# Kernel tuning notes

Measured on AMD Instinct MI355X. Metric: run time of the kernel, lower is better.

Reference implementation:

```python
import jax, jax.numpy as jnp
import numpy as np

RADIUS = 0.2
NSAMPLE = 32
NPOINT = 2048
EPS = 1e-5


def setup_inputs() -> dict:
    key = jax.random.key(0)
    ks = jax.random.split(key, 6)
    B, N, C = 8, 8192, 64
    xyz = jax.random.uniform(ks[0], (B, N, 3), dtype=jnp.float32)
    features = jax.random.normal(ks[1], (B, C, N), dtype=jnp.float32)
    W1 = jax.random.normal(ks[2], (64, 67), dtype=jnp.float32) * 0.1
    W2 = jax.random.normal(ks[3], (64, 64), dtype=jnp.float32) * 0.1
    W3 = jax.random.normal(ks[4], (128, 64), dtype=jnp.float32) * 0.1
    return {
        'xyz': xyz, 'features': features,
        'W1': W1, 'g1': jnp.ones((64,), jnp.float32), 'b1': jnp.zeros((64,), jnp.float32),
        'W2': W2, 'g2': jnp.ones((64,), jnp.float32), 'b2': jnp.zeros((64,), jnp.float32),
        'W3': W3, 'g3': jnp.ones((128,), jnp.float32), 'b3': jnp.zeros((128,), jnp.float32),
    }


def furthest_point_sample(xyz, npoint):
    # xyz: (B, N, 3) -> (B, npoint) int32 indices, first index is 0 (CUDA FPS convention)
    B, N, _ = xyz.shape
    idxs0 = jnp.zeros((B, npoint), dtype=jnp.int32)
    dists0 = jnp.full((B, N), 1e10, dtype=xyz.dtype)
    last0 = jnp.zeros((B,), dtype=jnp.int32)

    def body(i, state):
        idxs, dists, last = state
        last_pt = xyz[jnp.arange(B), last]                      # (B, 3)
        d = jnp.sum((xyz - last_pt[:, None, :]) ** 2, axis=-1)  # (B, N)
        dists = jnp.minimum(dists, d)
        nxt = jnp.argmax(dists, axis=-1).astype(jnp.int32)
        idxs = idxs.at[:, i].set(nxt)
        return (idxs, dists, nxt)

    idxs, _, _ = jax.lax.fori_loop(1, npoint, body, (idxs0, dists0, last0))
    return idxs


def ball_query(xyz, new_xyz, radius, nsample):
    # Returns (B, S, nsample) int32: first `nsample` points within radius of each
    # query center, padded with the first in-ball index (pointnet2 convention).
    N = xyz.shape[1]
    d2 = jnp.sum((new_xyz[:, :, None, :] - xyz[:, None, :, :]) ** 2, axis=-1)  # (B,S,N)
    key = jnp.where(d2 < radius * radius, jnp.arange(N, dtype=jnp.int32), N)
    neg_vals, _ = jax.lax.top_k(-key, nsample)   # k smallest keys = earliest in-ball indices
    cand = -neg_vals                             # (B, S, nsample)
    first = cand[..., :1]
    return jnp.where(cand < N, cand, first)


def reference(xyz, features, W1, g1, b1, W2, g2, b2, W3, g3, b3):
    B = xyz.shape[0]
    fps_idx = furthest_point_sample(xyz, NPOINT)              # (B, S)
    new_xyz = xyz[jnp.arange(B)[:, None], fps_idx]            # (B, S, 3)

    idx = ball_query(xyz, new_xyz, RADIUS, NSAMPLE)           # (B, S, ns)
    bb = jnp.arange(B)[:, None, None]
    grouped_xyz = xyz[bb, idx] - new_xyz[:, :, None, :]       # (B, S, ns, 3) relative coords
    grouped_f = features.transpose(0, 2, 1)[bb, idx]          # (B, S, ns, C)
    g = jnp.concatenate([grouped_xyz, grouped_f], axis=-1)    # (B, S, ns, 3+C)
    g = g.transpose(0, 3, 1, 2)                               # (B, 3+C, S, ns)

    for W, ga, be in ((W1, g1, b1), (W2, g2, b2), (W3, g3, b3)):
        h = jnp.einsum('oc,bcsn->bosn', W, g)                 # 1x1 conv
        mu = h.mean(axis=(0, 2, 3), keepdims=True)            # training-mode BN stats
        var = h.var(axis=(0, 2, 3), keepdims=True)
        h = (h - mu) / jnp.sqrt(var + EPS)
        g = jax.nn.relu(h * ga[None, :, None, None] + be[None, :, None, None])

    feats = g.max(axis=-1)                                    # (B, mlp[-1], S)
    return new_xyz, feats
```

## Files before the change

### kernel.cpp

```cpp
#include <hip/hip_runtime.h>
#include <hip/hip_bf16.h>
#include <stdint.h>

#define NB 8
#define NN 8192
#define NC 64
#define NS 2048
#define NK 32
#define NCOL (NB*NS*NK)

typedef float v2f __attribute__((ext_vector_type(2)));

__device__ __forceinline__ unsigned short f2bf(float x) {
    union { float f; unsigned u; } c; c.f = x;
    unsigned r = c.u + 0x7fffu + ((c.u >> 16) & 1u);
    return (unsigned short)(r >> 16);
}
__device__ __forceinline__ float bf2f(unsigned v16) {
    union { float f; unsigned u; } c; c.u = v16 << 16;
    return c.f;
}

template<int CTRL>
__device__ __forceinline__ unsigned long long dpp_max_u64(unsigned long long key) {
    int olo = __builtin_amdgcn_update_dpp(0, (int)(unsigned)key,        CTRL, 0xf, 0xf, true);
    int ohi = __builtin_amdgcn_update_dpp(0, (int)(unsigned)(key >> 32), CTRL, 0xf, 0xf, true);
    unsigned long long ok = ((unsigned long long)(unsigned)ohi << 32) | (unsigned)olo;
    return ok > key ? ok : key;
}
template<int CTRL>
__device__ __forceinline__ float dpp_add_f32(float x) {
    int o = __builtin_amdgcn_update_dpp(0, __float_as_int(x), CTRL, 0xf, 0xf, true);
    return x + __int_as_float(o);
}
template<int CTRL>
__device__ __forceinline__ float dpp_max_f32(float x) {
    int o = __builtin_amdgcn_update_dpp(__float_as_int(x), __float_as_int(x), CTRL, 0xf, 0xf, false);
    return fmaxf(x, __int_as_float(o));
}
template<int CTRL>
__device__ __forceinline__ float dpp_min_f32(float x) {
    int o = __builtin_amdgcn_update_dpp(__float_as_int(x), __float_as_int(x), CTRL, 0xf, 0xf, false);
    return fminf(x, __int_as_float(o));
}
template<int CTRL>
__device__ __forceinline__ unsigned dpp_max_u32(unsigned x) {
    int o = __builtin_amdgcn_update_dpp((int)x, (int)x, CTRL, 0xf, 0xf, false);
    unsigned ou = (unsigned)o;
    return x > ou ? x : ou;
}
template<int CTRL, int RM>
__device__ __forceinline__ unsigned dpp_add_u32(unsigned x) {
    int o = __builtin_amdgcn_update_dpp(0, (int)x, CTRL, RM, 0xf, true);
    return x + (unsigned)o;
}
__device__ __forceinline__ float wave_red_min(float x) {
    x = dpp_min_f32<0x111>(x); x = dpp_min_f32<0x112>(x);
    x = dpp_min_f32<0x114>(x); x = dpp_min_f32<0x118>(x);
    x = dpp_min_f32<0x142>(x); x = dpp_min_f32<0x143>(x);
    return __int_as_float(__builtin_amdgcn_readlane(__float_as_int(x), 63));
}
__device__ __forceinline__ float wave_red_max(float x) {
    x = dpp_max_f32<0x111>(x); x = dpp_max_f32<0x112>(x);
    x = dpp_max_f32<0x114>(x); x = dpp_max_f32<0x118>(x);
    x = dpp_max_f32<0x142>(x); x = dpp_max_f32<0x143>(x);
    return __int_as_float(__builtin_amdgcn_readlane(__float_as_int(x), 63));
}
__device__ __forceinline__ v2f relu2(v2f v) {
    v.x = fmaxf(v.x, 0.f); v.y = fmaxf(v.y, 0.f); return v;
}

__device__ __forceinline__ unsigned expand_bits10(unsigned v) {
    v = (v * 0x00010001u) & 0xFF0000FFu;
    v = (v * 0x00000101u) & 0x0F00F00Fu;
    v = (v * 0x00000011u) & 0xC30C30C3u;
    v = (v * 0x00000005u) & 0x49249249u;
    return v;
}
__global__ __launch_bounds__(1024) void sort_kernel(const float* __restrict__ xyz,
    float4* __restrict__ sorted)
{
    __shared__ unsigned cnt[2048];
    __shared__ unsigned codes[NN];
    __shared__ unsigned wsum[16];
    const int b = blockIdx.x;
    const int tid = threadIdx.x;
    const int w = tid >> 6;
    const int lane = tid & 63;
    const float* xb = xyz + (size_t)b * NN * 3;
    cnt[tid] = 0; cnt[tid + 1024] = 0;
    __syncthreads();
    for (int p = tid; p < NN; p += 1024) {
        float x = xb[3*p+0], y = xb[3*p+1], z = xb[3*p+2];
        int qx = (int)(x * 1024.f); qx = qx < 0 ? 0 : (qx > 1023 ? 1023 : qx);
        int qy = (int)(y * 1024.f); qy = qy < 0 ? 0 : (qy > 1023 ? 1023 : qy);
        int qz = (int)(z * 1024.f); qz = qz < 0 ? 0 : (qz > 1023 ? 1023 : qz);
        unsigned m = expand_bits10((unsigned)qx)
                   | (expand_bits10((unsigned)qy) << 1)
                   | (expand_bits10((unsigned)qz) << 2);
        unsigned bk = m >> 19;
        codes[p] = bk;
        atomicAdd(&cnt[bk], 1u);
    }
    __syncthreads();
    unsigned c0 = cnt[2*tid], c1 = cnt[2*tid+1];
    unsigned s = c0 + c1;
    unsigned v = s;
    v = dpp_add_u32<0x111, 0xf>(v);
    v = dpp_add_u32<0x112, 0xf>(v);
    v = dpp_add_u32<0x114, 0xf>(v);
    v = dpp_add_u32<0x118, 0xf>(v);
    v = dpp_add_u32<0x142, 0xa>(v);
    v = dpp_add_u32<0x143, 0xc>(v);
    if (lane == 63) wsum[w] = v;
    __syncthreads();
    unsigned wbase = 0;
#pragma unroll
    for (int j = 0; j < 15; ++j) {
        unsigned t = wsum[j];
        wbase += (j < w) ? t : 0u;
    }
    unsigned excl = wbase + v - s;
    cnt[2*tid]   = excl;
    cnt[2*tid+1] = excl + c0;
    __syncthreads();
    for (int p = tid; p < NN; p += 1024) {
        unsigned bk = codes[p];
        unsigned pos = atomicAdd(&cnt[bk], 1u);
        float4 o;
        o.x = xb[3*p+0]; o.y = xb[3*p+1]; o.z = xb[3*p+2];
        o.w = __int_as_float(p);
        sorted[(size_t)b * NN + pos] = o;
    }
}

__global__ __launch_bounds__(1024) void fps_kernel(const float* __restrict__ xyz,
    const float4* __restrict__ sorted,
    float* __restrict__ new_xyz, float* __restrict__ out_newxyz)
{
#pragma clang fp contract(off)
    const int b = blockIdx.x;
    const int tid = threadIdx.x;
    const int w = tid >> 6;
    const int lane = tid & 63;
    __shared__ float sx[NN], sy[NN], sz[NN];
    __shared__ float s_hist[NS * 3];
    __shared__ unsigned long long s_key[2][16];
    const float4* sp = sorted + (size_t)b * NN + (size_t)w * 512 + lane;
    v2f px[4], py[4], pz[4], dmin[4];
    unsigned plo[8];
    float bnx = 1e30f, bny = 1e30f, bnz = 1e30f;
    float bxx = -1e30f, bxy = -1e30f, bxz = -1e30f;
#pragma unroll
    for (int m = 0; m < 4; ++m) {
        float4 a = sp[128*m];
        float4 c = sp[128*m + 64];
        px[m].x = a.x; px[m].y = c.x;
        py[m].x = a.y; py[m].y = c.y;
        pz[m].x = a.z; pz[m].y = c.z;
        dmin[m].x = 1e10f; dmin[m].y = 1e10f;
        int ia = __float_as_int(a.w), ic = __float_as_int(c.w);
        plo[2*m]   = ~(unsigned)ia;
        plo[2*m+1] = ~(unsigned)ic;
        sx[ia] = a.x; sy[ia] = a.y; sz[ia] = a.z;
        sx[ic] = c.x; sy[ic] = c.y; sz[ic] = c.z;
        bnx = fminf(bnx, fminf(a.x, c.x)); bxx = fmaxf(bxx, fmaxf(a.x, c.x));
        bny = fminf(bny, fminf(a.y, c.y)); bxy = fmaxf(bxy, fmaxf(a.y, c.y));
        bnz = fminf(bnz, fminf(a.z, c.z)); bxz = fmaxf(bxz, fmaxf(a.z, c.z));
    }
    bnx = wave_red_min(bnx); bny = wave_red_min(bny); bnz = wave_red_min(bnz);
    bxx = wave_red_max(bxx); bxy = wave_red_max(bxy); bxz = wave_red_max(bxz);

    const float* xb = xyz + (size_t)b * NN * 3;
    float lx = xb[0], ly = xb[1], lz = xb[2];
    if (tid == 0) { s_hist[0] = lx; s_hist[1] = ly; s_hist[2] = lz; }
    float ckv = 1e30f;
    unsigned cklo = 0u;
    __syncthreads();

    for (int i = 1; i < NS; ++i) {
        float cdx = fmaxf(fmaxf(bnx - lx, lx - bxx), 0.f);
        float cdy = fmaxf(fmaxf(bny - ly, ly - bxy), 0.f);
        float cdz = fmaxf(fmaxf(bnz - lz, lz - bxz), 0.f);
        float lb = (cdx*cdx + cdy*cdy) + cdz*cdz;
        if (!(lb >= ckv)) {
            v2f l2x; l2x.x = lx; l2x.y = lx;
            v2f l2y; l2y.x = ly; l2y.y = ly;
            v2f l2z; l2z.x = lz; l2z.y = lz;
#pragma unroll
            for (int m = 0; m < 4; ++m) {
                v2f dx = px[m] - l2x;
                v2f dy = py[m] - l2y;
                v2f dz = pz[m] - l2z;
                v2f d = (dx*dx + dy*dy) + dz*dz;
                dmin[m].x = fminf(dmin[m].x, d.x);
                dmin[m].y = fminf(dmin[m].y, d.y);
            }
            float bv = fmaxf(
                fmaxf(fmaxf(dmin[0].x, dmin[0].y), fmaxf(dmin[1].x, dmin[1].y)),
                fmaxf(fmaxf(dmin[2].x, dmin[2].y), fmaxf(dmin[3].x, dmin[3].y)));
            float mv = bv;
            mv = dpp_max_f32<0x111>(mv); mv = dpp_max_f32<0x112>(mv);
            mv = dpp_max_f32<0x114>(mv); mv = dpp_max_f32<0x118>(mv);
            mv = dpp_max_f32<0x142>(mv); mv = dpp_max_f32<0x143>(mv);
            const unsigned vmb = (unsigned)__builtin_amdgcn_readlane(__float_as_int(mv), 63);
            const float vmax = __uint_as_float(vmb);
            unsigned cand = 0u;
#pragma unroll
            for (int m = 0; m < 4; ++m) {
                unsigned t0 = (dmin[m].x == vmax) ? plo[2*m]   : 0u;
                unsigned t1 = (dmin[m].y == vmax) ? plo[2*m+1] : 0u;
                unsigned t = t0 > t1 ? t0 : t1;
                cand = cand > t ? cand : t;
            }
            cand = dpp_max_u32<0x111>(cand); cand = dpp_max_u32<0x112>(cand);
            cand = dpp_max_u32<0x114>(cand); cand = dpp_max_u32<0x118>(cand);
            cand = dpp_max_u32<0x142>(cand); cand = dpp_max_u32<0x143>(cand);
            cklo = (unsigned)__builtin_amdgcn_readlane((int)cand, 63);
            ckv = vmax;
        }
        if (lane == 0)
            s_key[i & 1][w] = ((unsigned long long)__float_as_uint(ckv) << 32) | cklo;
        __syncthreads();
        unsigned long long k = s_key[i & 1][lane & 15];
        k = dpp_max_u64<0x111>(k);
        k = dpp_max_u64<0x112>(k);
        k = dpp_max_u64<0x114>(k);
        k = dpp_max_u64<0x118>(k);
        const int ix = ~__builtin_amdgcn_readlane((int)(unsigned)(k & 0xffffffffull), 15);
        lx = sx[ix]; ly = sy[ix]; lz = sz[ix];
        if (tid == 0) {
            s_hist[3*i+0] = lx; s_hist[3*i+1] = ly; s_hist[3*i+2] = lz;
        }
    }
    __syncthreads();
    float* nw = new_xyz + (size_t)b * NS * 3;
    float* ow = out_newxyz + (size_t)b * NS * 3;
    for (int t = tid; t < NS * 3; t += 1024) {
        float v = s_hist[t];
        nw[t] = v; ow[t] = v;
    }
}

__global__ __launch_bounds__(256) void transpose_kernel(const float* __restrict__ f,
    float* __restrict__ ft)
{
    __shared__ float tile[64][65];
    int b = blockIdx.y;
    int p0 = blockIdx.x * 64;
    for (int k = threadIdx.x; k < 64*64; k += 256) {
        int c = k >> 6, p = k & 63;
        tile[c][p] = f[((size_t)b * NC + c) * NN + p0 + p];
    }
    __syncthreads();
    for (int k = threadIdx.x; k < 64*64; k += 256) {
        int p = k >> 6, c = k & 63;
        ft[((size_t)b * NN + p0 + p) * NC + c] = tile[c][p];
    }
}

__global__ __launch_bounds__(256) void ballquery_kernel(const float* __restrict__ xyz,
    const float* __restrict__ new_xyz, int* __restrict__ idx)
{
#pragma clang fp contract(off)
    const int q = blockIdx.x * 4 + (threadIdx.x >> 6);
    const int lane = threadIdx.x & 63;
    const int b = q >> 11;
    const float r2 = (float)(0.2 * 0.2);
    const float* xb = xyz + (size_t)b * NN * 3;
    const float* nx = new_xyz + (size_t)q * 3;
    float qx = nx[0], qy = nx[1], qz = nx[2];
    int cnt = 0, first = -1;
    int* out = idx + (size_t)q * NK;
    for (int base = 0; base < NN; base += 64) {
        int p = base + lane;
        float x = xb[p*3+0], y = xb[p*3+1], z = xb[p*3+2];
        float dx = qx - x, dy = qy - y, dz = qz - z;
        float d2 = (dx*dx + dy*dy) + dz*dz;
        bool in = d2 < r2;
        unsigned long long m = __ballot(in);
        if (m) {
            if (first < 0) first = base + __builtin_ctzll(m);
            if (in) {
                int rank = cnt + __popcll(m & ((1ull << lane) - 1ull));
                if (rank < NK) out[rank] = p;
            }
            cnt += __popcll(m);
            if (cnt >= NK) break;
        }
    }
    for (int k = cnt + lane; k < NK; k += 64) out[k] = first;
}

__global__ __launch_bounds__(256, 2) void layer1_kernel(const float* __restrict__ xyz,
    const float* __restrict__ new_xyz, const int* __restrict__ idx,
    const float* __restrict__ ft, const float* __restrict__ W1,
    unsigned short* __restrict__ h1)
{
    const int col = blockIdx.x * 256 + threadIdx.x;
    const int b = col >> 16;
    const int s = (col >> 5) & 2047;
    const int p = idx[col];
    v2f g[34];
    float* gf = (float*)g;
    {
        const float* nx = new_xyz + ((size_t)(b * NS + s)) * 3;
        const float* xp = xyz + ((size_t)(b * NN + p)) * 3;
        gf[0] = xp[0] - nx[0]; gf[1] = xp[1] - nx[1]; gf[2] = xp[2] - nx[2];
    }
    const float4* fp = (const float4*)(ft + ((size_t)(b * NN + p)) * NC);
#pragma unroll
    for (int c4 = 0; c4 < 16; ++c4) {
        float4 v = fp[c4];
        gf[3 + 4*c4 + 0] = v.x; gf[3 + 4*c4 + 1] = v.y;
        gf[3 + 4*c4 + 2] = v.z; gf[3 + 4*c4 + 3] = v.w;
    }
    gf[67] = 0.f;
    uint4* dst = (uint4*)(h1 + (size_t)col * 64);
#pragma unroll
    for (int half = 0; half < 2; ++half) {
        float h[32];
#pragma unroll 4
        for (int o16 = 0; o16 < 32; ++o16) {
            const float* w = W1 + (half*32 + o16) * 67;
            v2f acc; acc.x = 0.f; acc.y = 0.f;
#pragma unroll
            for (int k = 0; k < 33; ++k) {
                v2f wv; wv.x = w[2*k]; wv.y = w[2*k+1];
                acc = wv * g[k] + acc;
            }
            h[o16] = fmaf(w[66], gf[66], acc.x + acc.y);
        }
#pragma unroll
        for (int k = 0; k < 4; ++k) {
            uint4 v;
            v.x = (unsigned)f2bf(h[8*k+0]) | ((unsigned)f2bf(h[8*k+1]) << 16);
            v.y = (unsigned)f2bf(h[8*k+2]) | ((unsigned)f2bf(h[8*k+3]) << 16);
            v.z = (unsigned)f2bf(h[8*k+4]) | ((unsigned)f2bf(h[8*k+5]) << 16);
            v.w = (unsigned)f2bf(h[8*k+6]) | ((unsigned)f2bf(h[8*k+7]) << 16);
            dst[half*4 + k] = v;
        }
    }
}

__global__ __launch_bounds__(256) void stats_kernel(const unsigned short* __restrict__ h,
    float* __restrict__ sums)
{
    __shared__ float ls[64], lq[64];
    const int tid = threadIdx.x;
    if (tid < 64) { ls[tid] = 0.f; lq[tid] = 0.f; }
    __syncthreads();
    float s[8] = {0,0,0,0,0,0,0,0}, q[8] = {0,0,0,0,0,0,0,0};
    const int gt = blockIdx.x * 256 + tid;
    const int G = gridDim.x * 256;
    const uint4* src = (const uint4*)h;
    const int nvec = NCOL * 8;
    for (int i = gt; i < nvec; i += G) {
        uint4 v = src[i];
        float f0 = bf2f(v.x & 0xffffu), f1 = bf2f(v.x >> 16);
        float f2 = bf2f(v.y & 0xffffu), f3 = bf2f(v.y >> 16);
        float f4 = bf2f(v.z & 0xffffu), f5 = bf2f(v.z >> 16);
        float f6 = bf2f(v.w & 0xffffu), f7 = bf2f(v.w >> 16);
        s[0] += f0; q[0] = fmaf(f0, f0, q[0]);
        s[1] += f1; q[1] = fmaf(f1, f1, q[1]);
        s[2] += f2; q[2] = fmaf(f2, f2, q[2]);
        s[3] += f3; q[3] = fmaf(f3, f3, q[3]);
        s[4] += f4; q[4] = fmaf(f4, f4, q[4]);
        s[5] += f5; q[5] = fmaf(f5, f5, q[5]);
        s[6] += f6; q[6] = fmaf(f6, f6, q[6]);
        s[7] += f7; q[7] = fmaf(f7, f7, q[7]);
    }
    const int obase = (tid & 7) * 8;
#pragma unroll
    for (int j = 0; j < 8; ++j) {
        atomicAdd(&ls[obase + j], s[j]);
        atomicAdd(&lq[obase + j], q[j]);
    }
    __syncthreads();
    if (tid < 64) {
        atomicAdd(&sums[tid*2+0], ls[tid]);
        atomicAdd(&sums[tid*2+1], lq[tid]);
    }
}

__global__ void finalize_kernel(const float* __restrict__ sums,
    const float* __restrict__ gamma, const float* __restrict__ beta,
    float* __restrict__ ab, int nch)
{
    int c = threadIdx.x;
    if (c < nch) {
        const float invM = 1.0f / 524288.0f;
        float mu = sums[c*2] * invM;
        float var = sums[c*2+1] * invM - mu * mu;
        float a = gamma[c] / sqrtf(var + 1e-5f);
        ab[c] = a;
        ab[nch + c] = fmaf(-mu, a, beta[c]);
    }
}

__global__ __launch_bounds__(256, 2) void layer2_kernel(const unsigned short* __restrict__ h1,
    const float* __restrict__ ab1, const float* __restrict__ W2,
    unsigned short* __restrict__ h2)
{
    const int col = blockIdx.x * 256 + threadIdx.x;
    const uint4* src = (const uint4*)(h1 + (size_t)col * 64);
    v2f g[32];
    float* gf = (float*)g;
#pragma unroll
    for (int k = 0; k < 8; ++k) {
        uint4 v = src[k];
        gf[8*k+0] = bf2f(v.x & 0xffffu); gf[8*k+1] = bf2f(v.x >> 16);
        gf[8*k+2] = bf2f(v.y & 0xffffu); gf[8*k+3] = bf2f(v.y >> 16);
        gf[8*k+4] = bf2f(v.z & 0xffffu); gf[8*k+5] = bf2f(v.z >> 16);
        gf[8*k+6] = bf2f(v.w & 0xffffu); gf[8*k+7] = bf2f(v.w >> 16);
    }
    const v2f* a2 = (const v2f*)ab1;
    const v2f* b2 = (const v2f*)(ab1 + 64);
#pragma unroll
    for (int k = 0; k < 32; ++k)
        g[k] = relu2(a2[k] * g[k] + b2[k]);
    uint4* dst = (uint4*)(h2 + (size_t)col * 64);
#pragma unroll
    for (int half = 0; half < 2; ++half) {
        float h[32];
#pragma unroll 4
        for (int o16 = 0; o16 < 32; ++o16) {
            const float* w = W2 + ((half*32 + o16) << 6);
            v2f acc; acc.x = 0.f; acc.y = 0.f;
#pragma unroll
            for (int k = 0; k < 32; ++k) {
                v2f wv; wv.x = w[2*k]; wv.y = w[2*k+1];
                acc = wv * g[k] + acc;
            }
            h[o16] = acc.x + acc.y;
        }
#pragma unroll
        for (int k = 0; k < 4; ++k) {
            uint4 v;
            v.x = (unsigned)f2bf(h[8*k+0]) | ((unsigned)f2bf(h[8*k+1]) << 16);
            v.y = (unsigned)f2bf(h[8*k+2]) | ((unsigned)f2bf(h[8*k+3]) << 16);
            v.z = (unsigned)f2bf(h[8*k+4]) | ((unsigned)f2bf(h[8*k+5]) << 16);
            v.w = (unsigned)f2bf(h[8*k+6]) | ((unsigned)f2bf(h[8*k+7]) << 16);
            dst[half*4 + k] = v;
        }
    }
}

__global__ __launch_bounds__(256, 2) void layer3_kernel(const unsigned short* __restrict__ h2,
    const float* __restrict__ ab2, const float* __restrict__ W3,
    float* __restrict__ hmax, float* __restrict__ hmin, float* __restrict__ sums3)
{
    __shared__ float ls[128], lq[128];
    const int tid = threadIdx.x;
    if (tid < 128) { ls[tid] = 0.f; lq[tid] = 0.f; }
    __syncthreads();
    const int col = blockIdx.x * 256 + tid;
    const int q = col >> 5;
    const uint4* src = (const uint4*)(h2 + (size_t)col * 64);
    v2f g[32];
    float* gf = (float*)g;
#pragma unroll
    for (int k = 0; k < 8; ++k) {
        uint4 v = src[k];
        gf[8*k+0] = bf2f(v.x & 0xffffu); gf[8*k+1] = bf2f(v.x >> 16);
        gf[8*k+2] = bf2f(v.y & 0xffffu); gf[8*k+3] = bf2f(v.y >> 16);
        gf[8*k+4] = bf2f(v.z & 0xffffu); gf[8*k+5] = bf2f(v.z >> 16);
        gf[8*k+6] = bf2f(v.w & 0xffffu); gf[8*k+7] = bf2f(v.w >> 16);
    }
    const v2f* a2 = (const v2f*)ab2;
    const v2f* b2 = (const v2f*)(ab2 + 64);
#pragma unroll
    for (int k = 0; k < 32; ++k)
        g[k] = relu2(a2[k] * g[k] + b2[k]);
    const bool leader = ((tid & 31) == 31);
#pragma unroll 2
    for (int o = 0; o < 128; ++o) {
        const float* w = W3 + (o << 6);
        v2f acc; acc.x = 0.f; acc.y = 0.f;
#pragma unroll
        for (int k = 0; k < 32; ++k) {
            v2f wv; wv.x = w[2*k]; wv.y = w[2*k+1];
            acc = wv * g[k] + acc;
        }
        float hv = acc.x + acc.y;
        float sm = hv, sq = hv*hv, mx = hv, mn = hv;
        sm = dpp_add_f32<0x111>(sm); sq = dpp_add_f32<0x111>(sq);
        mx = dpp_max_f32<0x111>(mx); mn = dpp_min_f32<0x111>(mn);
        sm = dpp_add_f32<0x112>(sm); sq = dpp_add_f32<0x112>(sq);
        mx = dpp_max_f32<0x112>(mx); mn = dpp_min_f32<0x112>(mn);
        sm = dpp_add_f32<0x114>(sm); sq = dpp_add_f32<0x114>(sq);
        mx = dpp_max_f32<0x114>(mx); mn = dpp_min_f32<0x114>(mn);
        sm = dpp_add_f32<0x118>(sm); sq = dpp_add_f32<0x118>(sq);
        mx = dpp_max_f32<0x118>(mx); mn = dpp_min_f32<0x118>(mn);
        sm = dpp_add_f32<0x142>(sm); sq = dpp_add_f32<0x142>(sq);
        mx = dpp_max_f32<0x142>(mx); mn = dpp_min_f32<0x142>(mn);
        if (leader) {
            hmax[(size_t)o * 16384 + q] = mx;
            hmin[(size_t)o * 16384 + q] = mn;
            atomicAdd(&ls[o], sm);
            atomicAdd(&lq[o], sq);
        }
    }
    __syncthreads();
    if (tid < 128) {
        atomicAdd(&sums3[tid*2+0], ls[tid]);
        atomicAdd(&sums3[tid*2+1], lq[tid]);
    }
}

__global__ __launch_bounds__(256) void final_kernel(const float* __restrict__ hmax,
    const float* __restrict__ hmin, const float* __restrict__ ab3,
    float* __restrict__ out)
{
    const int t = blockIdx.x * 256 + threadIdx.x;
    const int s = t & 2047;
    const int o = (t >> 11) & 127;
    const int b = t >> 18;
    const int q = (b << 11) + s;
    float a = ab3[o], c = ab3[128 + o];
    float h = (a >= 0.f) ? hmax[(size_t)o * 16384 + q] : hmin[(size_t)o * 16384 + q];
    out[t] = fmaxf(fmaf(a, h, c), 0.f);
}

extern "C" void kernel_launch(void* const* d_in, const int* in_sizes, int n_in,
                              void* d_out, int out_size, void* d_ws, size_t ws_size,
                              hipStream_t stream) {
    (void)in_sizes; (void)n_in; (void)out_size; (void)ws_size;
    const float* xyz      = (const float*)d_in[0];
    const float* features = (const float*)d_in[1];
    const float* W1 = (const float*)d_in[2];
    const float* g1 = (const float*)d_in[3];
    const float* b1 = (const float*)d_in[4];
    const float* W2 = (const float*)d_in[5];
    const float* g2 = (const float*)d_in[6];
    const float* b2 = (const float*)d_in[7];
    const float* W3 = (const float*)d_in[8];
    const float* g3 = (const float*)d_in[9];
    const float* b3 = (const float*)d_in[10];

    char* ws = (char*)d_ws;
    float*          new_xyz = (float*)(ws + 0);
    int*            idx     = (int*)(ws + 196608);
    float*          ft      = (float*)(ws + 2293760);
    unsigned short* h1      = (unsigned short*)(ws + 19070976);
    unsigned short* h2      = (unsigned short*)(ws + 86179840);
    float*          hmax    = (float*)(ws + 153288704);
    float*          hmin    = (float*)(ws + 161677312);
    float*          sums    = (float*)(ws + 170065920);
    float*          ab      = (float*)(ws + 170067968);
    float* sums1 = sums;        float* ab1 = ab;
    float* sums2 = sums + 128;  float* ab2 = ab + 128;
    float* sums3 = sums + 256;  float* ab3 = ab + 256;

    float4* sorted = (float4*)h1;

    float* out_newxyz = (float*)d_out;
    float* out_feats  = (float*)d_out + 49152;

    hipMemsetAsync(sums, 0, 2048, stream);

    sort_kernel<<<NB, 1024, 0, stream>>>(xyz, sorted);
    fps_kernel<<<NB, 1024, 0, stream>>>(xyz, sorted, new_xyz, out_newxyz);
    transpose_kernel<<<dim3(NN/64, NB), 256, 0, stream>>>(features, ft);
    ballquery_kernel<<<(NB*NS)/4, 256, 0, stream>>>(xyz, new_xyz, idx);
    layer1_kernel<<<NCOL/256, 256, 0, stream>>>(xyz, new_xyz, idx, ft, W1, h1);
    stats_kernel<<<1024, 256, 0, stream>>>(h1, sums1);
    finalize_kernel<<<1, 128, 0, stream>>>(sums1, g1, b1, ab1, 64);
    layer2_kernel<<<NCOL/256, 256, 0, stream>>>(h1, ab1, W2, h2);
    stats_kernel<<<1024, 256, 0, stream>>>(h2, sums2);
    finalize_kernel<<<1, 128, 0, stream>>>(sums2, g2, b2, ab2, 64);
    layer3_kernel<<<NCOL/256, 256, 0, stream>>>(h2, ab2, W3, hmax, hmin, sums3);
    finalize_kernel<<<1, 128, 0, stream>>>(sums3, g3, b3, ab3, 128);
    final_kernel<<<(NB*128*NS)/256, 256, 0, stream>>>(hmax, hmin, ab3, out_feats);
}
```

Before: 2.261 ms.

## Halve FPS block to 8 waves and carry winner coordinates in wave records

The FPS kernel now runs with 512 threads (8 waves), each lane holding 16 points instead of 8. Each wave looks up its own candidate's coordinates inside its bounding-box-gated branch and publishes value, index and xyz in a shared record. The cross-wave reduction then needs only 3 DPP steps over 8 entries and reads the winner's coordinates via readlane, instead of a dependent LDS lookup after the barrier. This shortens the serial per-iteration critical path and barrier cost, at the price of more per-lane work and register pressure. Ties are broken by index first and then by wave id packed into the low bits.

```diff
diff --git a/kernel.cpp b/kernel.cpp
--- a/kernel.cpp
+++ b/kernel.cpp
@@ -8,6 +8,7 @@
 #define NS 2048
 #define NK 32
 #define NCOL (NB*NS*NK)
+#define FW 8
 
 typedef float v2f __attribute__((ext_vector_type(2)));
 
@@ -21,13 +22,6 @@
     return c.f;
 }
 
-template<int CTRL>
-__device__ __forceinline__ unsigned long long dpp_max_u64(unsigned long long key) {
-    int olo = __builtin_amdgcn_update_dpp(0, (int)(unsigned)key,        CTRL, 0xf, 0xf, true);
-    int ohi = __builtin_amdgcn_update_dpp(0, (int)(unsigned)(key >> 32), CTRL, 0xf, 0xf, true);
-    unsigned long long ok = ((unsigned long long)(unsigned)ohi << 32) | (unsigned)olo;
-    return ok > key ? ok : key;
-}
 template<int CTRL>
 __device__ __forceinline__ float dpp_add_f32(float x) {
     int o = __builtin_amdgcn_update_dpp(0, __float_as_int(x), CTRL, 0xf, 0xf, true);
@@ -134,7 +128,7 @@
     }
 }
 
-__global__ __launch_bounds__(1024) void fps_kernel(const float* __restrict__ xyz,
+__global__ __launch_bounds__(512) void fps_kernel(const float* __restrict__ xyz,
     const float4* __restrict__ sorted,
     float* __restrict__ new_xyz, float* __restrict__ out_newxyz)
 {
@@ -145,14 +139,14 @@
     const int lane = tid & 63;
     __shared__ float sx[NN], sy[NN], sz[NN];
     __shared__ float s_hist[NS * 3];
-    __shared__ unsigned long long s_key[2][16];
-    const float4* sp = sorted + (size_t)b * NN + (size_t)w * 512 + lane;
-    v2f px[4], py[4], pz[4], dmin[4];
-    unsigned plo[8];
+    __shared__ float s_rec[2][FW][12];
+    const float4* sp = sorted + (size_t)b * NN + (size_t)w * 1024 + lane;
+    v2f px[8], py[8], pz[8], dmin[8];
+    unsigned plo[16];
     float bnx = 1e30f, bny = 1e30f, bnz = 1e30f;
     float bxx = -1e30f, bxy = -1e30f, bxz = -1e30f;
 #pragma unroll
-    for (int m = 0; m < 4; ++m) {
+    for (int m = 0; m < 8; ++m) {
         float4 a = sp[128*m];
         float4 c = sp[128*m + 64];
         px[m].x = a.x; px[m].y = c.x;
@@ -171,11 +165,20 @@
     bnx = wave_red_min(bnx); bny = wave_red_min(bny); bnz = wave_red_min(bnz);
     bxx = wave_red_max(bxx); bxy = wave_red_max(bxy); bxz = wave_red_max(bxz);
 
+    int rw, roff;
+    if (lane < 8)       { rw = lane;      roff = 0; }
+    else if (lane < 16) { rw = lane - 8;  roff = 2; }
+    else if (lane < 24) { rw = lane - 16; roff = 4; }
+    else                { rw = 0;         roff = 0; }
+    const float* rb0 = &s_rec[0][rw][roff];
+    const float* rb1 = &s_rec[1][rw][roff];
+
     const float* xb = xyz + (size_t)b * NN * 3;
     float lx = xb[0], ly = xb[1], lz = xb[2];
     if (tid == 0) { s_hist[0] = lx; s_hist[1] = ly; s_hist[2] = lz; }
     float ckv = 1e30f;
-    unsigned cklo = 0u;
+    unsigned cki = 0u;
+    float cwx = 0.f, cwy = 0.f, cwz = 0.f;
     __syncthreads();
 
     for (int i = 1; i < NS; ++i) {
@@ -188,7 +191,7 @@
             v2f l2y; l2y.x = ly; l2y.y = ly;
             v2f l2z; l2z.x = lz; l2z.y = lz;
 #pragma unroll
-            for (int m = 0; m < 4; ++m) {
+            for (int m = 0; m < 8; ++m) {
                 v2f dx = px[m] - l2x;
                 v2f dy = py[m] - l2y;
                 v2f dz = pz[m] - l2z;
@@ -196,39 +199,55 @@
                 dmin[m].x = fminf(dmin[m].x, d.x);
                 dmin[m].y = fminf(dmin[m].y, d.y);
             }
-            float bv = fmaxf(
-                fmaxf(fmaxf(dmin[0].x, dmin[0].y), fmaxf(dmin[1].x, dmin[1].y)),
-                fmaxf(fmaxf(dmin[2].x, dmin[2].y), fmaxf(dmin[3].x, dmin[3].y)));
-            float mv = bv;
+            float t0 = fmaxf(fmaxf(dmin[0].x, dmin[0].y), fmaxf(dmin[1].x, dmin[1].y));
+            float t1 = fmaxf(fmaxf(dmin[2].x, dmin[2].y), fmaxf(dmin[3].x, dmin[3].y));
+            float t2 = fmaxf(fmaxf(dmin[4].x, dmin[4].y), fmaxf(dmin[5].x, dmin[5].y));
+            float t3 = fmaxf(fmaxf(dmin[6].x, dmin[6].y), fmaxf(dmin[7].x, dmin[7].y));
+            float mv = fmaxf(fmaxf(t0, t1), fmaxf(t2, t3));
             mv = dpp_max_f32<0x111>(mv); mv = dpp_max_f32<0x112>(mv);
             mv = dpp_max_f32<0x114>(mv); mv = dpp_max_f32<0x118>(mv);
             mv = dpp_max_f32<0x142>(mv); mv = dpp_max_f32<0x143>(mv);
-            const unsigned vmb = (unsigned)__builtin_amdgcn_readlane(__float_as_int(mv), 63);
-            const float vmax = __uint_as_float(vmb);
+            const float vmax = __uint_as_float(
+                (unsigned)__builtin_amdgcn_readlane(__float_as_int(mv), 63));
             unsigned cand = 0u;
 #pragma unroll
-            for (int m = 0; m < 4; ++m) {
-                unsigned t0 = (dmin[m].x == vmax) ? plo[2*m]   : 0u;
-                unsigned t1 = (dmin[m].y == vmax) ? plo[2*m+1] : 0u;
-                unsigned t = t0 > t1 ? t0 : t1;
-                cand = cand > t ? cand : t;
+            for (int m = 0; m < 8; ++m) {
+                unsigned u0 = (dmin[m].x == vmax) ? plo[2*m]   : 0u;
+                unsigned u1 = (dmin[m].y == vmax) ? plo[2*m+1] : 0u;
+                unsigned u = u0 > u1 ? u0 : u1;
+                cand = cand > u ? cand : u;
             }
             cand = dpp_max_u32<0x111>(cand); cand = dpp_max_u32<0x112>(cand);
             cand = dpp_max_u32<0x114>(cand); cand = dpp_max_u32<0x118>(cand);
             cand = dpp_max_u32<0x142>(cand); cand = dpp_max_u32<0x143>(cand);
-            cklo = (unsigned)__builtin_amdgcn_readlane((int)cand, 63);
+            cki = (unsigned)__builtin_amdgcn_readlane((int)cand, 63);
             ckv = vmax;
-        }
-        if (lane == 0)
-            s_key[i & 1][w] = ((unsigned long long)__float_as_uint(ckv) << 32) | cklo;
+            const int ix = (int)(~cki);
+            cwx = sx[ix]; cwy = sy[ix]; cwz = sz[ix];
+        }
+        if (lane == 63) {
+            float* r = (float*)&s_rec[i & 1][w][0];
+            ((unsigned*)r)[0] = __float_as_uint(ckv);
+            ((unsigned*)r)[1] = (cki << 3) | (unsigned)w;
+            r[2] = cwx; r[3] = cwy; r[4] = cwz;
+        }
         __syncthreads();
-        unsigned long long k = s_key[i & 1][lane & 15];
-        k = dpp_max_u64<0x111>(k);
-        k = dpp_max_u64<0x112>(k);
-        k = dpp_max_u64<0x114>(k);
-        k = dpp_max_u64<0x118>(k);
-        const int ix = ~__builtin_amdgcn_readlane((int)(unsigned)(k & 0xffffffffull), 15);
-        lx = sx[ix]; ly = sy[ix]; lz = sz[ix];
+        const float* rp = (i & 1) ? rb1 : rb0;
+        uint2 rec = *(const uint2*)rp;
+        float kv = __uint_as_float(rec.x);
+        float m1 = kv;
+        m1 = dpp_max_f32<0x111>(m1); m1 = dpp_max_f32<0x112>(m1);
+        m1 = dpp_max_f32<0x114>(m1);
+        const float gmax = __uint_as_float(
+            (unsigned)__builtin_amdgcn_readlane(__float_as_int(m1), 7));
+        unsigned c = (lane < 8 && kv == gmax) ? rec.y : 0u;
+        c = dpp_max_u32<0x111>(c); c = dpp_max_u32<0x112>(c);
+        c = dpp_max_u32<0x114>(c);
+        const unsigned kwin = (unsigned)__builtin_amdgcn_readlane((int)c, 7);
+        const int wstar = (int)(kwin & 7u);
+        lx = __uint_as_float((unsigned)__builtin_amdgcn_readlane((int)rec.x, 8 + wstar));
+        ly = __uint_as_float((unsigned)__builtin_amdgcn_readlane((int)rec.y, 8 + wstar));
+        lz = __uint_as_float((unsigned)__builtin_amdgcn_readlane((int)rec.x, 16 + wstar));
         if (tid == 0) {
             s_hist[3*i+0] = lx; s_hist[3*i+1] = ly; s_hist[3*i+2] = lz;
         }
@@ -236,7 +255,7 @@
     __syncthreads();
     float* nw = new_xyz + (size_t)b * NS * 3;
     float* ow = out_newxyz + (size_t)b * NS * 3;
-    for (int t = tid; t < NS * 3; t += 1024) {
+    for (int t = tid; t < NS * 3; t += 512) {
         float v = s_hist[t];
         nw[t] = v; ow[t] = v;
     }
@@ -560,7 +579,7 @@
     hipMemsetAsync(sums, 0, 2048, stream);
 
     sort_kernel<<<NB, 1024, 0, stream>>>(xyz, sorted);
-    fps_kernel<<<NB, 1024, 0, stream>>>(xyz, sorted, new_xyz, out_newxyz);
+    fps_kernel<<<NB, 512, 0, stream>>>(xyz, sorted, new_xyz, out_newxyz);
     transpose_kernel<<<dim3(NN/64, NB), 256, 0, stream>>>(features, ft);
     ballquery_kernel<<<(NB*NS)/4, 256, 0, stream>>>(xyz, new_xyz, idx);
     layer1_kernel<<<NCOL/256, 256, 0, stream>>>(xyz, new_xyz, idx, ft, W1, h1);
```

Result: slower. 2.532 ms (+12.0%).

## Pack two batches per FPS block with 8 waves each and register-held winner coords

Applied to the files above, without the earlier changes.

The FPS kernel now processes two batches per 1024-thread block, so each batch gets 8 waves instead of 16, and each wave holds 1024 points split into two spatially-sorted sub-chunks, each with its own bounding-box prune. The winning point's coordinates are written by the owning lane into a small shared record and broadcast with readlane. This replaces the full 8192-point shared coordinate table and the 64-bit key reduction with a two-pass 32-bit max. The aim is fewer blocks and barriers, finer-grained pruning, and less shared-memory traffic per iteration. In exchange each wave does twice the serial work per iteration, only 4 blocks run, and batches sharing a block are coupled through __syncthreads.

```diff
diff --git a/kernel.cpp b/kernel.cpp
--- a/kernel.cpp
+++ b/kernel.cpp
@@ -21,13 +21,6 @@
     return c.f;
 }
 
-template<int CTRL>
-__device__ __forceinline__ unsigned long long dpp_max_u64(unsigned long long key) {
-    int olo = __builtin_amdgcn_update_dpp(0, (int)(unsigned)key,        CTRL, 0xf, 0xf, true);
-    int ohi = __builtin_amdgcn_update_dpp(0, (int)(unsigned)(key >> 32), CTRL, 0xf, 0xf, true);
-    unsigned long long ok = ((unsigned long long)(unsigned)ohi << 32) | (unsigned)olo;
-    return ok > key ? ok : key;
-}
 template<int CTRL>
 __device__ __forceinline__ float dpp_add_f32(float x) {
     int o = __builtin_amdgcn_update_dpp(0, __float_as_int(x), CTRL, 0xf, 0xf, true);
@@ -134,110 +127,161 @@
     }
 }
 
+#define VMAX6(mv) \
+    mv = dpp_max_f32<0x111>(mv); mv = dpp_max_f32<0x112>(mv); \
+    mv = dpp_max_f32<0x114>(mv); mv = dpp_max_f32<0x118>(mv); \
+    mv = dpp_max_f32<0x142>(mv); mv = dpp_max_f32<0x143>(mv);
+#define UMAX6(cv) \
+    cv = dpp_max_u32<0x111>(cv); cv = dpp_max_u32<0x112>(cv); \
+    cv = dpp_max_u32<0x114>(cv); cv = dpp_max_u32<0x118>(cv); \
+    cv = dpp_max_u32<0x142>(cv); cv = dpp_max_u32<0x143>(cv);
+#define UPD(M) \
+    dx = px[M]-l2x; dy = py[M]-l2y; dz = pz[M]-l2z; \
+    d = (dx*dx + dy*dy) + dz*dz; \
+    dmin[M].x = fminf(dmin[M].x, d.x); dmin[M].y = fminf(dmin[M].y, d.y);
+#define TIE(M) \
+    u = (dmin[M].x == vmax) ? (pidx[M] & 0xffffu) : 0u; cand = cand > u ? cand : u; \
+    u = (dmin[M].y == vmax) ? (pidx[M] >> 16)     : 0u; cand = cand > u ? cand : u;
+#define CSEL(S, M) \
+    e = ((pidx[M] & 0xffffu) == cki##S); iwin##S = iwin##S | e; \
+    wx##S = e ? px[M].x : wx##S; wy##S = e ? py[M].x : wy##S; wz##S = e ? pz[M].x : wz##S; \
+    e = ((pidx[M] >> 16) == cki##S);     iwin##S = iwin##S | e; \
+    wx##S = e ? px[M].y : wx##S; wy##S = e ? py[M].y : wy##S; wz##S = e ? pz[M].y : wz##S;
+#define DO_SUB(S, MA, MB, MC, MD) \
+  { \
+    float cdx = fmaxf(fmaxf(bn##S##x - lx, lx - bx##S##x), 0.f); \
+    float cdy = fmaxf(fmaxf(bn##S##y - ly, ly - bx##S##y), 0.f); \
+    float cdz = fmaxf(fmaxf(bn##S##z - lz, lz - bx##S##z), 0.f); \
+    float lb = (cdx*cdx + cdy*cdy) + cdz*cdz; \
+    if (!(lb >= ckv##S)) {                        \
+      v2f l2x; l2x.x = lx; l2x.y = lx; \
+      v2f l2y; l2y.x = ly; l2y.y = ly; \
+      v2f l2z; l2z.x = lz; l2z.y = lz; \
+      v2f dx, dy, dz, d; \
+      UPD(MA) UPD(MB) UPD(MC) UPD(MD) \
+      float t0 = fmaxf(fmaxf(dmin[MA].x, dmin[MA].y), fmaxf(dmin[MB].x, dmin[MB].y)); \
+      float t1 = fmaxf(fmaxf(dmin[MC].x, dmin[MC].y), fmaxf(dmin[MD].x, dmin[MD].y)); \
+      float mv = fmaxf(t0, t1); \
+      VMAX6(mv) \
+      const float vmax = __uint_as_float( \
+          (unsigned)__builtin_amdgcn_readlane(__float_as_int(mv), 63)); \
+      unsigned cand = 0u, u; \
+      TIE(MA) TIE(MB) TIE(MC) TIE(MD) \
+      UMAX6(cand) \
+      cki##S = (unsigned)__builtin_amdgcn_readlane((int)cand, 63); \
+      ckv##S = vmax; \
+      iwin##S = false;                           \
+      bool e; \
+      CSEL(S, MA) CSEL(S, MB) CSEL(S, MC) CSEL(S, MD) \
+    } \
+    if (lane == 0) { \
+      uint2 kk2; kk2.x = __float_as_uint(ckv##S); kk2.y = (cki##S << 4) | (unsigned)sid##S; \
+      W->kvki[sid##S] = kk2; \
+    } \
+    if (iwin##S) { \
+      W->coord[sid##S]      = wx##S; \
+      W->coord[16 + sid##S] = wy##S; \
+      W->coord[32 + sid##S] = wz##S; \
+    } \
+  }
+
+struct FpsRec { uint2 kvki[16]; float coord[48]; };
+
 __global__ __launch_bounds__(1024) void fps_kernel(const float* __restrict__ xyz,
     const float4* __restrict__ sorted,
     float* __restrict__ new_xyz, float* __restrict__ out_newxyz)
 {
 #pragma clang fp contract(off)
-    const int b = blockIdx.x;
+    const int blk = blockIdx.x;
     const int tid = threadIdx.x;
     const int w = tid >> 6;
     const int lane = tid & 63;
-    __shared__ float sx[NN], sy[NN], sz[NN];
-    __shared__ float s_hist[NS * 3];
-    __shared__ unsigned long long s_key[2][16];
-    const float4* sp = sorted + (size_t)b * NN + (size_t)w * 512 + lane;
-    v2f px[4], py[4], pz[4], dmin[4];
-    unsigned plo[8];
-    float bnx = 1e30f, bny = 1e30f, bnz = 1e30f;
-    float bxx = -1e30f, bxy = -1e30f, bxz = -1e30f;
-#pragma unroll
-    for (int m = 0; m < 4; ++m) {
+    const int bbl = w >> 3;
+    const int ww = w & 7;
+    const int batch = blk * 2 + bbl;
+
+    __shared__ FpsRec s_rec[2][2];
+    __shared__ float s_hist[2][NS * 3];
+
+    const float4* sp = sorted + (size_t)batch * NN + (size_t)ww * 1024 + lane;
+    v2f px[8], py[8], pz[8], dmin[8];
+    unsigned pidx[8];
+    float bn0x = 1e30f, bn0y = 1e30f, bn0z = 1e30f;
+    float bx0x = -1e30f, bx0y = -1e30f, bx0z = -1e30f;
+    float bn1x = 1e30f, bn1y = 1e30f, bn1z = 1e30f;
+    float bx1x = -1e30f, bx1y = -1e30f, bx1z = -1e30f;
+#pragma unroll
+    for (int m = 0; m < 8; ++m) {
         float4 a = sp[128*m];
         float4 c = sp[128*m + 64];
         px[m].x = a.x; px[m].y = c.x;
         py[m].x = a.y; py[m].y = c.y;
         pz[m].x = a.z; pz[m].y = c.z;
         dmin[m].x = 1e10f; dmin[m].y = 1e10f;
-        int ia = __float_as_int(a.w), ic = __float_as_int(c.w);
-        plo[2*m]   = ~(unsigned)ia;
-        plo[2*m+1] = ~(unsigned)ic;
-        sx[ia] = a.x; sy[ia] = a.y; sz[ia] = a.z;
-        sx[ic] = c.x; sy[ic] = c.y; sz[ic] = c.z;
-        bnx = fminf(bnx, fminf(a.x, c.x)); bxx = fmaxf(bxx, fmaxf(a.x, c.x));
-        bny = fminf(bny, fminf(a.y, c.y)); bxy = fmaxf(bxy, fmaxf(a.y, c.y));
-        bnz = fminf(bnz, fminf(a.z, c.z)); bxz = fmaxf(bxz, fmaxf(a.z, c.z));
-    }
-    bnx = wave_red_min(bnx); bny = wave_red_min(bny); bnz = wave_red_min(bnz);
-    bxx = wave_red_max(bxx); bxy = wave_red_max(bxy); bxz = wave_red_max(bxz);
-
-    const float* xb = xyz + (size_t)b * NN * 3;
+        unsigned ia = (unsigned)__float_as_int(a.w), ic = (unsigned)__float_as_int(c.w);
+        pidx[m] = (8192u - ia) | ((8192u - ic) << 16);
+        if (m < 4) {
+            bn0x = fminf(bn0x, fminf(a.x, c.x)); bx0x = fmaxf(bx0x, fmaxf(a.x, c.x));
+            bn0y = fminf(bn0y, fminf(a.y, c.y)); bx0y = fmaxf(bx0y, fmaxf(a.y, c.y));
+            bn0z = fminf(bn0z, fminf(a.z, c.z)); bx0z = fmaxf(bx0z, fmaxf(a.z, c.z));
+        } else {
+            bn1x = fminf(bn1x, fminf(a.x, c.x)); bx1x = fmaxf(bx1x, fmaxf(a.x, c.x));
+            bn1y = fminf(bn1y, fminf(a.y, c.y)); bx1y = fmaxf(bx1y, fmaxf(a.y, c.y));
+            bn1z = fminf(bn1z, fminf(a.z, c.z)); bx1z = fmaxf(bx1z, fmaxf(a.z, c.z));
+        }
+    }
+    bn0x = wave_red_min(bn0x); bn0y = wave_red_min(bn0y); bn0z = wave_red_min(bn0z);
+    bx0x = wave_red_max(bx0x); bx0y = wave_red_max(bx0y); bx0z = wave_red_max(bx0z);
+    bn1x = wave_red_min(bn1x); bn1y = wave_red_min(bn1y); bn1z = wave_red_min(bn1z);
+    bx1x = wave_red_max(bx1x); bx1y = wave_red_max(bx1y); bx1z = wave_red_max(bx1z);
+
+    const int roff = (lane < 16) ? lane * 8 : 128 + (lane - 16) * 4;
+    const char* rb0 = (const char*)&s_rec[0][bbl] + roff;
+    const char* rb1 = (const char*)&s_rec[1][bbl] + roff;
+
+    const float* xb = xyz + (size_t)batch * NN * 3;
     float lx = xb[0], ly = xb[1], lz = xb[2];
-    if (tid == 0) { s_hist[0] = lx; s_hist[1] = ly; s_hist[2] = lz; }
-    float ckv = 1e30f;
-    unsigned cklo = 0u;
-    __syncthreads();
+    if (lane == 0 && ww == 0) {
+        s_hist[bbl][0] = lx; s_hist[bbl][1] = ly; s_hist[bbl][2] = lz;
+    }
+    float ckv0 = 1e30f, ckv1 = 1e30f;
+    unsigned cki0 = 0u, cki1 = 0u;
+    bool iwin0 = false, iwin1 = false;
+    float wx0 = 0, wy0 = 0, wz0 = 0, wx1 = 0, wy1 = 0, wz1 = 0;
+    const int sid0 = ww * 2, sid1 = ww * 2 + 1;
 
     for (int i = 1; i < NS; ++i) {
-        float cdx = fmaxf(fmaxf(bnx - lx, lx - bxx), 0.f);
-        float cdy = fmaxf(fmaxf(bny - ly, ly - bxy), 0.f);
-        float cdz = fmaxf(fmaxf(bnz - lz, lz - bxz), 0.f);
-        float lb = (cdx*cdx + cdy*cdy) + cdz*cdz;
-        if (!(lb >= ckv)) {
-            v2f l2x; l2x.x = lx; l2x.y = lx;
-            v2f l2y; l2y.x = ly; l2y.y = ly;
-            v2f l2z; l2z.x = lz; l2z.y = lz;
-#pragma unroll
-            for (int m = 0; m < 4; ++m) {
-                v2f dx = px[m] - l2x;
-                v2f dy = py[m] - l2y;
-                v2f dz = pz[m] - l2z;
-                v2f d = (dx*dx + dy*dy) + dz*dz;
-                dmin[m].x = fminf(dmin[m].x, d.x);
-                dmin[m].y = fminf(dmin[m].y, d.y);
-            }
-            float bv = fmaxf(
-                fmaxf(fmaxf(dmin[0].x, dmin[0].y), fmaxf(dmin[1].x, dmin[1].y)),
-                fmaxf(fmaxf(dmin[2].x, dmin[2].y), fmaxf(dmin[3].x, dmin[3].y)));
-            float mv = bv;
-            mv = dpp_max_f32<0x111>(mv); mv = dpp_max_f32<0x112>(mv);
-            mv = dpp_max_f32<0x114>(mv); mv = dpp_max_f32<0x118>(mv);
-            mv = dpp_max_f32<0x142>(mv); mv = dpp_max_f32<0x143>(mv);
-            const unsigned vmb = (unsigned)__builtin_amdgcn_readlane(__float_as_int(mv), 63);
-            const float vmax = __uint_as_float(vmb);
-            unsigned cand = 0u;
-#pragma unroll
-            for (int m = 0; m < 4; ++m) {
-                unsigned t0 = (dmin[m].x == vmax) ? plo[2*m]   : 0u;
-                unsigned t1 = (dmin[m].y == vmax) ? plo[2*m+1] : 0u;
-                unsigned t = t0 > t1 ? t0 : t1;
-                cand = cand > t ? cand : t;
-            }
-            cand = dpp_max_u32<0x111>(cand); cand = dpp_max_u32<0x112>(cand);
-            cand = dpp_max_u32<0x114>(cand); cand = dpp_max_u32<0x118>(cand);
-            cand = dpp_max_u32<0x142>(cand); cand = dpp_max_u32<0x143>(cand);
-            cklo = (unsigned)__builtin_amdgcn_readlane((int)cand, 63);
-            ckv = vmax;
-        }
-        if (lane == 0)
-            s_key[i & 1][w] = ((unsigned long long)__float_as_uint(ckv) << 32) | cklo;
+        FpsRec* W = &s_rec[i & 1][bbl];
+        DO_SUB(0, 0, 1, 2, 3)
+        DO_SUB(1, 4, 5, 6, 7)
         __syncthreads();
-        unsigned long long k = s_key[i & 1][lane & 15];
-        k = dpp_max_u64<0x111>(k);
-        k = dpp_max_u64<0x112>(k);
-        k = dpp_max_u64<0x114>(k);
-        k = dpp_max_u64<0x118>(k);
-        const int ix = ~__builtin_amdgcn_readlane((int)(unsigned)(k & 0xffffffffull), 15);
-        lx = sx[ix]; ly = sy[ix]; lz = sz[ix];
-        if (tid == 0) {
-            s_hist[3*i+0] = lx; s_hist[3*i+1] = ly; s_hist[3*i+2] = lz;
-        }
-    }
-    __syncthreads();
-    float* nw = new_xyz + (size_t)b * NS * 3;
-    float* ow = out_newxyz + (size_t)b * NS * 3;
-    for (int t = tid; t < NS * 3; t += 1024) {
-        float v = s_hist[t];
+        const char* rp = (i & 1) ? rb1 : rb0;
+        uint2 kk; kk.x = 0u; kk.y = 0u;
+        unsigned rcbits = 0u;
+        if (lane < 16) kk = *(const uint2*)rp;
+        else rcbits = *(const unsigned*)rp;
+        unsigned mkv = (lane < 16) ? kk.x : 0u;
+        mkv = dpp_max_u32<0x111>(mkv); mkv = dpp_max_u32<0x112>(mkv);
+        mkv = dpp_max_u32<0x114>(mkv); mkv = dpp_max_u32<0x118>(mkv);
+        const unsigned gkv = (unsigned)__builtin_amdgcn_readlane((int)mkv, 15);
+        unsigned c = (lane < 16 && kk.x == gkv) ? kk.y : 0u;
+        c = dpp_max_u32<0x111>(c); c = dpp_max_u32<0x112>(c);
+        c = dpp_max_u32<0x114>(c); c = dpp_max_u32<0x118>(c);
+        const unsigned kwin = (unsigned)__builtin_amdgcn_readlane((int)c, 15);
+        const int sub = (int)(kwin & 15u);
+        lx = __uint_as_float((unsigned)__builtin_amdgcn_readlane((int)rcbits, 16 + sub));
+        ly = __uint_as_float((unsigned)__builtin_amdgcn_readlane((int)rcbits, 32 + sub));
+        lz = __uint_as_float((unsigned)__builtin_amdgcn_readlane((int)rcbits, 48 + sub));
+        if (lane == 0 && ww == 0) {
+            s_hist[bbl][3*i+0] = lx; s_hist[bbl][3*i+1] = ly; s_hist[bbl][3*i+2] = lz;
+        }
+    }
+    __syncthreads();
+    const float* hf = (const float*)s_hist;
+    float* nw = new_xyz + (size_t)(blk * 2) * NS * 3;
+    float* ow = out_newxyz + (size_t)(blk * 2) * NS * 3;
+    for (int t = tid; t < 2 * NS * 3; t += 1024) {
+        float v = hf[t];
         nw[t] = v; ow[t] = v;
     }
 }
@@ -560,7 +604,7 @@
     hipMemsetAsync(sums, 0, 2048, stream);
 
     sort_kernel<<<NB, 1024, 0, stream>>>(xyz, sorted);
-    fps_kernel<<<NB, 1024, 0, stream>>>(xyz, sorted, new_xyz, out_newxyz);
+    fps_kernel<<<NB/2, 1024, 0, stream>>>(xyz, sorted, new_xyz, out_newxyz);
     transpose_kernel<<<dim3(NN/64, NB), 256, 0, stream>>>(features, ft);
     ballquery_kernel<<<(NB*NS)/4, 256, 0, stream>>>(xyz, new_xyz, idx);
     layer1_kernel<<<NCOL/256, 256, 0, stream>>>(xyz, new_xyz, idx, ft, W1, h1);
```

New measurement: 5.659 ms. 150% more time.

## Have each wave publish its winner coordinates instead of staging all points in LDS

Applied to the files above, without the earlier changes.

FPS no longer copies all 8192 points into shared-memory coordinate arrays. Each wave now publishes its winning distance, a packed index key and the winner's xyz in a small double-buffered record. Wave 0 reduces the 16 records with 32-bit DPP max and readlanes, then writes the chosen point to the history buffer. Every thread reads the new point back after a second barrier. This removes the 64-bit key reduction and the large LDS footprint, but adds a second __syncthreads per iteration and serialises the cross-wave reduction through wave 0.

```diff
diff --git a/kernel.cpp b/kernel.cpp
--- a/kernel.cpp
+++ b/kernel.cpp
@@ -21,13 +21,6 @@
     return c.f;
 }
 
-template<int CTRL>
-__device__ __forceinline__ unsigned long long dpp_max_u64(unsigned long long key) {
-    int olo = __builtin_amdgcn_update_dpp(0, (int)(unsigned)key,        CTRL, 0xf, 0xf, true);
-    int ohi = __builtin_amdgcn_update_dpp(0, (int)(unsigned)(key >> 32), CTRL, 0xf, 0xf, true);
-    unsigned long long ok = ((unsigned long long)(unsigned)ohi << 32) | (unsigned)olo;
-    return ok > key ? ok : key;
-}
 template<int CTRL>
 __device__ __forceinline__ float dpp_add_f32(float x) {
     int o = __builtin_amdgcn_update_dpp(0, __float_as_int(x), CTRL, 0xf, 0xf, true);
@@ -134,6 +127,17 @@
     }
 }
 
+#define VMAX6(mv) \
+    mv = dpp_max_f32<0x111>(mv); mv = dpp_max_f32<0x112>(mv); \
+    mv = dpp_max_f32<0x114>(mv); mv = dpp_max_f32<0x118>(mv); \
+    mv = dpp_max_f32<0x142>(mv); mv = dpp_max_f32<0x143>(mv);
+#define UMAX6(cv) \
+    cv = dpp_max_u32<0x111>(cv); cv = dpp_max_u32<0x112>(cv); \
+    cv = dpp_max_u32<0x114>(cv); cv = dpp_max_u32<0x118>(cv); \
+    cv = dpp_max_u32<0x142>(cv); cv = dpp_max_u32<0x143>(cv);
+
+struct FpsRec { uint2 kvki[16]; float coord[48]; };
+
 __global__ __launch_bounds__(1024) void fps_kernel(const float* __restrict__ xyz,
     const float4* __restrict__ sorted,
     float* __restrict__ new_xyz, float* __restrict__ out_newxyz)
@@ -143,12 +147,13 @@
     const int tid = threadIdx.x;
     const int w = tid >> 6;
     const int lane = tid & 63;
-    __shared__ float sx[NN], sy[NN], sz[NN];
+
+    __shared__ FpsRec s_rec[2];
     __shared__ float s_hist[NS * 3];
-    __shared__ unsigned long long s_key[2][16];
+
     const float4* sp = sorted + (size_t)b * NN + (size_t)w * 512 + lane;
     v2f px[4], py[4], pz[4], dmin[4];
-    unsigned plo[8];
+    unsigned pidx[4];
     float bnx = 1e30f, bny = 1e30f, bnz = 1e30f;
     float bxx = -1e30f, bxy = -1e30f, bxz = -1e30f;
 #pragma unroll
@@ -159,26 +164,30 @@
         py[m].x = a.y; py[m].y = c.y;
         pz[m].x = a.z; pz[m].y = c.z;
         dmin[m].x = 1e10f; dmin[m].y = 1e10f;
-        int ia = __float_as_int(a.w), ic = __float_as_int(c.w);
-        plo[2*m]   = ~(unsigned)ia;
-        plo[2*m+1] = ~(unsigned)ic;
-        sx[ia] = a.x; sy[ia] = a.y; sz[ia] = a.z;
-        sx[ic] = c.x; sy[ic] = c.y; sz[ic] = c.z;
+        unsigned ia = (unsigned)__float_as_int(a.w), ic = (unsigned)__float_as_int(c.w);
+        pidx[m] = (8192u - ia) | ((8192u - ic) << 16);
         bnx = fminf(bnx, fminf(a.x, c.x)); bxx = fmaxf(bxx, fmaxf(a.x, c.x));
         bny = fminf(bny, fminf(a.y, c.y)); bxy = fmaxf(bxy, fmaxf(a.y, c.y));
         bnz = fminf(bnz, fminf(a.z, c.z)); bxz = fmaxf(bxz, fmaxf(a.z, c.z));
     }
     bnx = wave_red_min(bnx); bny = wave_red_min(bny); bnz = wave_red_min(bnz);
     bxx = wave_red_max(bxx); bxy = wave_red_max(bxy); bxz = wave_red_max(bxz);
+
+    const int roff = (lane < 16) ? lane * 8 : 128 + (lane - 16) * 4;
+    const char* rb0 = (const char*)&s_rec[0] + roff;
+    const char* rb1 = (const char*)&s_rec[1] + roff;
 
     const float* xb = xyz + (size_t)b * NN * 3;
     float lx = xb[0], ly = xb[1], lz = xb[2];
     if (tid == 0) { s_hist[0] = lx; s_hist[1] = ly; s_hist[2] = lz; }
     float ckv = 1e30f;
-    unsigned cklo = 0u;
+    unsigned cki = 0u;
+    bool iwin = false;
+    float wx = 0.f, wy = 0.f, wz = 0.f;
     __syncthreads();
 
     for (int i = 1; i < NS; ++i) {
+        FpsRec* W = &s_rec[i & 1];
         float cdx = fmaxf(fmaxf(bnx - lx, lx - bxx), 0.f);
         float cdy = fmaxf(fmaxf(bny - ly, ly - bxy), 0.f);
         float cdz = fmaxf(fmaxf(bnz - lz, lz - bxz), 0.f);
@@ -196,42 +205,65 @@
                 dmin[m].x = fminf(dmin[m].x, d.x);
                 dmin[m].y = fminf(dmin[m].y, d.y);
             }
-            float bv = fmaxf(
-                fmaxf(fmaxf(dmin[0].x, dmin[0].y), fmaxf(dmin[1].x, dmin[1].y)),
-                fmaxf(fmaxf(dmin[2].x, dmin[2].y), fmaxf(dmin[3].x, dmin[3].y)));
-            float mv = bv;
-            mv = dpp_max_f32<0x111>(mv); mv = dpp_max_f32<0x112>(mv);
-            mv = dpp_max_f32<0x114>(mv); mv = dpp_max_f32<0x118>(mv);
-            mv = dpp_max_f32<0x142>(mv); mv = dpp_max_f32<0x143>(mv);
-            const unsigned vmb = (unsigned)__builtin_amdgcn_readlane(__float_as_int(mv), 63);
-            const float vmax = __uint_as_float(vmb);
-            unsigned cand = 0u;
+            float t0 = fmaxf(fmaxf(dmin[0].x, dmin[0].y), fmaxf(dmin[1].x, dmin[1].y));
+            float t1 = fmaxf(fmaxf(dmin[2].x, dmin[2].y), fmaxf(dmin[3].x, dmin[3].y));
+            float mv = fmaxf(t0, t1);
+            VMAX6(mv)
+            const float vmax = __uint_as_float(
+                (unsigned)__builtin_amdgcn_readlane(__float_as_int(mv), 63));
+            unsigned cand = 0u, u;
 #pragma unroll
             for (int m = 0; m < 4; ++m) {
-                unsigned t0 = (dmin[m].x == vmax) ? plo[2*m]   : 0u;
-                unsigned t1 = (dmin[m].y == vmax) ? plo[2*m+1] : 0u;
-                unsigned t = t0 > t1 ? t0 : t1;
-                cand = cand > t ? cand : t;
+                u = (dmin[m].x == vmax) ? (pidx[m] & 0xffffu) : 0u; cand = cand > u ? cand : u;
+                u = (dmin[m].y == vmax) ? (pidx[m] >> 16)     : 0u; cand = cand > u ? cand : u;
             }
-            cand = dpp_max_u32<0x111>(cand); cand = dpp_max_u32<0x112>(cand);
-            cand = dpp_max_u32<0x114>(cand); cand = dpp_max_u32<0x118>(cand);
-            cand = dpp_max_u32<0x142>(cand); cand = dpp_max_u32<0x143>(cand);
-            cklo = (unsigned)__builtin_amdgcn_readlane((int)cand, 63);
+            UMAX6(cand)
+            cki = (unsigned)__builtin_amdgcn_readlane((int)cand, 63);
             ckv = vmax;
-        }
-        if (lane == 0)
-            s_key[i & 1][w] = ((unsigned long long)__float_as_uint(ckv) << 32) | cklo;
+            iwin = false;
+            bool e;
+#pragma unroll
+            for (int m = 0; m < 4; ++m) {
+                e = ((pidx[m] & 0xffffu) == cki); iwin = iwin | e;
+                wx = e ? px[m].x : wx; wy = e ? py[m].x : wy; wz = e ? pz[m].x : wz;
+                e = ((pidx[m] >> 16) == cki);     iwin = iwin | e;
+                wx = e ? px[m].y : wx; wy = e ? py[m].y : wy; wz = e ? pz[m].y : wz;
+            }
+        }
+        if (lane == 0) {
+            uint2 kk2; kk2.x = __float_as_uint(ckv); kk2.y = (cki << 4) | (unsigned)w;
+            W->kvki[w] = kk2;
+        }
+        if (iwin) {
+            W->coord[w]      = wx;
+            W->coord[16 + w] = wy;
+            W->coord[32 + w] = wz;
+        }
         __syncthreads();
-        unsigned long long k = s_key[i & 1][lane & 15];
-        k = dpp_max_u64<0x111>(k);
-        k = dpp_max_u64<0x112>(k);
-        k = dpp_max_u64<0x114>(k);
-        k = dpp_max_u64<0x118>(k);
-        const int ix = ~__builtin_amdgcn_readlane((int)(unsigned)(k & 0xffffffffull), 15);
-        lx = sx[ix]; ly = sy[ix]; lz = sz[ix];
-        if (tid == 0) {
-            s_hist[3*i+0] = lx; s_hist[3*i+1] = ly; s_hist[3*i+2] = lz;
-        }
+        if (w == 0) {
+            const char* rp = (i & 1) ? rb1 : rb0;
+            uint2 kk; kk.x = 0u; kk.y = 0u;
+            unsigned rcbits = 0u;
+            if (lane < 16) kk = *(const uint2*)rp;
+            else rcbits = *(const unsigned*)rp;
+            unsigned mkv = (lane < 16) ? kk.x : 0u;
+            mkv = dpp_max_u32<0x111>(mkv); mkv = dpp_max_u32<0x112>(mkv);
+            mkv = dpp_max_u32<0x114>(mkv); mkv = dpp_max_u32<0x118>(mkv);
+            const unsigned gkv = (unsigned)__builtin_amdgcn_readlane((int)mkv, 15);
+            unsigned c = (lane < 16 && kk.x == gkv) ? kk.y : 0u;
+            c = dpp_max_u32<0x111>(c); c = dpp_max_u32<0x112>(c);
+            c = dpp_max_u32<0x114>(c); c = dpp_max_u32<0x118>(c);
+            const unsigned kwin = (unsigned)__builtin_amdgcn_readlane((int)c, 15);
+            const int sub = (int)(kwin & 15u);
+            float nx = __uint_as_float((unsigned)__builtin_amdgcn_readlane((int)rcbits, 16 + sub));
+            float ny = __uint_as_float((unsigned)__builtin_amdgcn_readlane((int)rcbits, 32 + sub));
+            float nz = __uint_as_float((unsigned)__builtin_amdgcn_readlane((int)rcbits, 48 + sub));
+            if (lane == 0) {
+                s_hist[3*i+0] = nx; s_hist[3*i+1] = ny; s_hist[3*i+2] = nz;
+            }
+        }
+        __syncthreads();
+        lx = s_hist[3*i+0]; ly = s_hist[3*i+1]; lz = s_hist[3*i+2];
     }
     __syncthreads();
     float* nw = new_xyz + (size_t)b * NS * 3;
```

Result: slower. 2.836 ms (+25.4%).
